# Optimization experiments

Measured on AMD Instinct MI355X. Metric: run time of the kernel, lower is better.

Reference implementation:

```python
import jax, jax.numpy as jnp
import numpy as np

N, E, F, H, G = 50000, 600000, 128, 128, 256
EPS = 1e-5
NEG_SLOPE = 0.2


def setup_inputs() -> dict:
    key = jax.random.key(0)
    ks = jax.random.split(key, 20)
    def w(k, shape, fan_in):
        return jax.random.normal(k, shape, jnp.float32) / np.sqrt(fan_in)
    x = jax.random.normal(ks[0], (N, F), jnp.float32)
    edge_index = jax.random.randint(ks[1], (2, E), 0, N, jnp.int32)
    batch = jnp.sort(jax.random.randint(ks[2], (N,), 0, G, jnp.int32))
    return {
        "x": x, "edge_index": edge_index, "batch": batch,
        "W1": w(ks[3], (F, H), F), "b1": jnp.zeros((H,), jnp.float32),
        "g1": jnp.ones((H,), jnp.float32), "be1": jnp.zeros((H,), jnp.float32),
        "Wg": w(ks[4], (H, H), H), "att_src": w(ks[5], (H,), H),
        "att_dst": w(ks[6], (H,), H), "bg": jnp.zeros((H,), jnp.float32),
        "g2": jnp.ones((H,), jnp.float32), "be2": jnp.zeros((H,), jnp.float32),
        "W3": w(ks[7], (H, H), H), "b3": jnp.zeros((H,), jnp.float32),
        "g3": jnp.ones((H,), jnp.float32), "be3": jnp.zeros((H,), jnp.float32),
        "fw1": w(ks[8], (H, H), H), "fb1": jnp.zeros((H,), jnp.float32),
        "fw2": w(ks[9], (H, 1), H), "fb2": jnp.zeros((1,), jnp.float32),
    }


def _with_self_loops(edge_index):
    loop = jnp.arange(N, dtype=edge_index.dtype)
    src = jnp.concatenate([edge_index[0], loop])
    dst = jnp.concatenate([edge_index[1], loop])
    return src, dst


def gcn_conv(x, W, b, src, dst):
    h = x @ W                                      # [N,H]
    deg = jax.ops.segment_sum(jnp.ones_like(dst, jnp.float32), dst, num_segments=N)
    dis = jnp.where(deg > 0, jax.lax.rsqrt(jnp.maximum(deg, 1.0)), 0.0)
    norm = dis[src] * dis[dst]                     # [E+N]
    msg = h[src] * norm[:, None]
    return jax.ops.segment_sum(msg, dst, num_segments=N) + b


def gat_conv(x, W, a_src, a_dst, b, src, dst):
    # single-head PyG GATConv with self loops
    h = x @ W                                      # [N,H]
    al_s = h @ a_src                               # [N]
    al_d = h @ a_dst
    e = jax.nn.leaky_relu(al_s[src] + al_d[dst], NEG_SLOPE)   # [E+N]
    m = jax.ops.segment_max(e, dst, num_segments=N)
    ex = jnp.exp(e - m[dst])
    denom = jax.ops.segment_sum(ex, dst, num_segments=N)
    alpha = ex / denom[dst]
    out = jax.ops.segment_sum(h[src] * alpha[:, None], dst, num_segments=N)
    return out + b


def batch_norm(x, gamma, beta):
    mu = jnp.mean(x, axis=0)
    var = jnp.var(x, axis=0)
    return gamma * (x - mu) * jax.lax.rsqrt(var + EPS) + beta


def reference(x, edge_index, batch, W1, b1, g1, be1, Wg, att_src, att_dst, bg,
              g2, be2, W3, b3, g3, be3, fw1, fb1, fw2, fb2):
    src, dst = _with_self_loops(edge_index)
    h = jax.nn.relu(batch_norm(gcn_conv(x, W1, b1, src, dst), g1, be1))
    # dropout = identity (eval mode)
    h = jax.nn.relu(batch_norm(gat_conv(h, Wg, att_src, att_dst, bg, src, dst), g2, be2))
    h = jax.nn.relu(batch_norm(gcn_conv(h, W3, b3, src, dst), g3, be3))
    # global mean pool over graphs
    sums = jax.ops.segment_sum(h, batch, num_segments=G)           # [G,H]
    cnts = jax.ops.segment_sum(jnp.ones((h.shape[0],), h.dtype), batch, num_segments=G)
    pooled = sums / jnp.maximum(cnts, 1.0)[:, None]
    z = jax.nn.relu(pooled @ fw1 + fb1)
    return z @ fw2 + fb2                                            # [G,1]
```

## Files before the change

### kernel.cpp

```cpp
#include <hip/hip_runtime.h>
#include <hip/hip_fp16.h>
#include <cstdint>

#define N_NODES 50000
#define N_EDGES 600000
#define HDIM    128
#define NGRAPH  256
#define EPSBN   1e-5f
#define NEG     0.2f
#define SCAN_B  196

__device__ __forceinline__ float lrelu(float v){ return v > 0.f ? v : NEG*v; }

typedef _Float16 f16x8 __attribute__((ext_vector_type(8)));
typedef float    f32x4 __attribute__((ext_vector_type(4)));

__global__ void prep_kernel(const float* __restrict__ W1, const float* __restrict__ Wg,
                            const float* __restrict__ W3, __half* __restrict__ Wt1,
                            __half* __restrict__ Wtg, __half* __restrict__ Wt3,
                            const int* __restrict__ ei, int* __restrict__ degi,
                            const int* __restrict__ batch, int* __restrict__ start){
  int b = blockIdx.x;
  if (b < 192){
    const float* W = (b < 64) ? W1 : (b < 128 ? Wg : W3);
    __half*     Wt = (b < 64) ? Wt1 : (b < 128 ? Wtg : Wt3);
    int idx = (b & 63)*256 + threadIdx.x;
    int k = idx >> 7, n = idx & 127;
    int kc = k >> 5, q = (k >> 3) & 3, j = k & 7;
    int nt = n >> 4, c16 = n & 15;
    Wt[(((kc*8 + nt)*4 + q)*16 + c16)*8 + j] = __float2half(W[idx]);
  } else if (b < 192 + 2344){
    int e = (b - 192)*256 + threadIdx.x;
    if (e < N_EDGES) atomicAdd(&degi[ei[N_EDGES + e]], 1);
  } else {
    int i = (b - 192 - 2344)*256 + threadIdx.x;
    if (i >= N_NODES) return;
    int bb = batch[i];
    int p = (i == 0) ? -1 : batch[i-1];
    for (int g = p+1; g <= bb; ++g) start[g] = i;
    if (i == N_NODES-1)
      for (int g = bb+1; g <= NGRAPH; ++g) start[g] = N_NODES;
  }
}

template<bool BN, bool F32IN, bool ATT, bool SCALE>
__global__ __launch_bounds__(256) void gemm_mfma(const void* __restrict__ Xv,
    const __half* __restrict__ Wt,
    const float* __restrict__ S, const float* __restrict__ Q,
    const float* __restrict__ gam, const float* __restrict__ bet,
    __half* __restrict__ Yh,
    const float* __restrict__ asr, const float* __restrict__ adt,
    float* __restrict__ al_s, float* __restrict__ al_d,
    const float* __restrict__ dis){
  __shared__ _Float16 scl[128], shl[128];
  const int t    = threadIdx.x;
  if (BN){
    if (t < 128){
      float mean = S[t] * (1.f/(float)N_NODES);
      float var  = fmaxf(Q[t]*(1.f/(float)N_NODES) - mean*mean, 0.f);
      float scale = gam[t]*rsqrtf(var + EPSBN);
      float shift = bet[t] - mean*scale;
      scl[t] = (_Float16)scale;
      shl[t] = (_Float16)shift;
    }
    __syncthreads();
  }
  const int wave = t >> 6, lane = t & 63;
  const int q    = lane >> 4, c16 = lane & 15;
  const int m0   = blockIdx.x*64 + wave*16;
  const int row  = m0 + c16;
  const int arow = (row > N_NODES-1) ? N_NODES-1 : row;

  f32x4 acc[8];
#pragma unroll
  for (int i = 0; i < 8; ++i) acc[i] = (f32x4){0.f,0.f,0.f,0.f};

  const f16x8* Wt8 = (const f16x8*)Wt;

#pragma unroll
  for (int kc = 0; kc < 4; ++kc){
    const int kof = kc*32 + q*8;
    f16x8 a;
    if (F32IN){
      const float* xp = (const float*)Xv + (long)arow*128 + kof;
      float4 x0 = *(const float4*)xp;
      float4 x1 = *(const float4*)(xp + 4);
      a[0]=(_Float16)x0.x; a[1]=(_Float16)x0.y; a[2]=(_Float16)x0.z; a[3]=(_Float16)x0.w;
      a[4]=(_Float16)x1.x; a[5]=(_Float16)x1.y; a[6]=(_Float16)x1.z; a[7]=(_Float16)x1.w;
    } else {
      f16x8 raw = *(const f16x8*)((const _Float16*)Xv + (long)arow*128 + kof);
      if (BN){
        f16x8 scv = *(const f16x8*)(scl + kof);
        f16x8 shv = *(const f16x8*)(shl + kof);
#pragma unroll
        for (int i = 0; i < 8; ++i){
          _Float16 v = (_Float16)(raw[i]*scv[i] + shv[i]);
          a[i] = v > (_Float16)0 ? v : (_Float16)0;
        }
      } else {
        a = raw;
      }
    }
#pragma unroll
    for (int nt = 0; nt < 8; ++nt){
      f16x8 b = Wt8[(kc*8 + nt)*64 + lane];
      acc[nt] = __builtin_amdgcn_mfma_f32_16x16x32_f16(b, a, acc[nt], 0, 0, 0);
    }
  }
  float rs = SCALE ? dis[arow] : 1.f;
  if (row < N_NODES){
    __half* yp = Yh + (long)row*128 + q*4;
#pragma unroll
    for (int nt = 0; nt < 8; ++nt){
      union { uint2 u; __half2 h[2]; } pk;
      pk.h[0] = __floats2half2_rn(acc[nt][0]*rs, acc[nt][1]*rs);
      pk.h[1] = __floats2half2_rn(acc[nt][2]*rs, acc[nt][3]*rs);
      *(uint2*)(yp + nt*16) = pk.u;
    }
  }
  if (ATT){
    float s = 0.f, d = 0.f;
#pragma unroll
    for (int nt = 0; nt < 8; ++nt){
      float4 av = *(const float4*)(asr + nt*16 + q*4);
      float4 bv = *(const float4*)(adt + nt*16 + q*4);
      s += acc[nt][0]*av.x + acc[nt][1]*av.y + acc[nt][2]*av.z + acc[nt][3]*av.w;
      d += acc[nt][0]*bv.x + acc[nt][1]*bv.y + acc[nt][2]*bv.z + acc[nt][3]*bv.w;
    }
    s += __shfl_xor(s, 16); s += __shfl_xor(s, 32);
    d += __shfl_xor(d, 16); d += __shfl_xor(d, 32);
    if (q == 0 && row < N_NODES){ al_s[row] = s; al_d[row] = d; }
  }
}

__global__ void scan_partial(const int* __restrict__ degi, int* __restrict__ part,
                             float* __restrict__ dis){
  __shared__ int sm[256];
  int t = threadIdx.x; int i = blockIdx.x*256 + t;
  int v = (i < N_NODES) ? degi[i] : 0;
  if (i < N_NODES) dis[i] = rsqrtf((float)v + 1.f);
  sm[t] = v;
  __syncthreads();
  for (int off = 128; off; off >>= 1){
    if (t < off) sm[t] += sm[t + off];
    __syncthreads();
  }
  if (t == 0) part[blockIdx.x] = sm[0];
}
__global__ void scan_final(const int* __restrict__ degi, const int* __restrict__ part,
                           int* __restrict__ rowp, int* __restrict__ work){
  __shared__ int sm[256];
  __shared__ int offs;
  int t = threadIdx.x; int i = blockIdx.x*256 + t;
  int pv = (t < SCAN_B && t < blockIdx.x) ? part[t] : 0;
  sm[t] = pv; __syncthreads();
  for (int off = 128; off; off >>= 1){
    if (t < off) sm[t] += sm[t + off];
    __syncthreads();
  }
  if (t == 0) offs = sm[0];
  __syncthreads();
  int v = (i < N_NODES) ? degi[i] : 0;
  sm[t] = v; __syncthreads();
  for (int off = 1; off < 256; off <<= 1){
    int add = (t >= off) ? sm[t - off] : 0;
    __syncthreads();
    sm[t] += add; __syncthreads();
  }
  if (i < N_NODES){
    int r = offs + sm[t] - v;
    rowp[i] = r;
    work[i] = r;
  }
}
__global__ void csr_scatter(const int* __restrict__ ei, int* __restrict__ work,
                            int* __restrict__ colx){
  int e = blockIdx.x*256 + threadIdx.x;
  if (e >= N_EDGES) return;
  int s = ei[e], d = ei[N_EDGES + e];
  int pos = atomicAdd(&work[d], 1);
  colx[pos] = s;
}

__global__ __launch_bounds__(256) void gcn_agg(const _Float16* __restrict__ Ah,
    const float* __restrict__ dis, const int* __restrict__ rowp,
    const int* __restrict__ degi, const int* __restrict__ colx,
    __half* __restrict__ Bh){
  const int n = blockIdx.x*4 + (threadIdx.x >> 6);
  const int lane = threadIdx.x & 63;
  const int g = lane >> 4, p = lane & 15;
  float acc[8] = {0,0,0,0,0,0,0,0};
  if (g == 0){
    f16x8 self = *(const f16x8*)(Ah + (long)n*128 + p*8);
#pragma unroll
    for (int i = 0; i < 8; ++i) acc[i] = (float)self[i];
  }
  const int e0 = rowp[n], cnt = degi[n];
  for (int base = 0; base < cnt; base += 64){
    int idx = base + lane;
    int s = 0; float w = 0.f;
    if (idx < cnt){ s = colx[e0 + idx]; w = 1.f; }
    int nit = min(64, cnt - base);
    int j = 0;
    for (; j + 8 <= nit; j += 8){
      int   s0 = __shfl(s, j + g),      s1 = __shfl(s, j + 4 + g);
      float w0 = __shfl(w, j + g),      w1 = __shfl(w, j + 4 + g);
      f16x8 r0 = *(const f16x8*)(Ah + (long)s0*128 + p*8);
      f16x8 r1 = *(const f16x8*)(Ah + (long)s1*128 + p*8);
#pragma unroll
      for (int i = 0; i < 8; ++i) acc[i] += w0 * (float)r0[i];
#pragma unroll
      for (int i = 0; i < 8; ++i) acc[i] += w1 * (float)r1[i];
    }
    for (; j < nit; j += 4){
      int   sj = __shfl(s, j + g);
      float wj = __shfl(w, j + g);
      f16x8 r = *(const f16x8*)(Ah + (long)sj*128 + p*8);
#pragma unroll
      for (int i = 0; i < 8; ++i) acc[i] += wj * (float)r[i];
    }
  }
#pragma unroll
  for (int i = 0; i < 8; ++i){
    acc[i] += __shfl_xor(acc[i], 16);
    acc[i] += __shfl_xor(acc[i], 32);
  }
  if (g == 0){
    float dn = dis[n];
    union { uint4 u; __half2 h[4]; } pk;
#pragma unroll
    for (int i = 0; i < 4; ++i)
      pk.h[i] = __floats2half2_rn(acc[2*i]*dn, acc[2*i+1]*dn);
    *(uint4*)(Bh + (long)n*128 + p*8) = pk.u;
  }
}

__global__ __launch_bounds__(256) void gat_agg(const _Float16* __restrict__ Ah,
    const float* __restrict__ al_s, const float* __restrict__ al_d,
    const int* __restrict__ rowp, const int* __restrict__ degi,
    const int* __restrict__ colx, __half* __restrict__ Bh){
  const int n = blockIdx.x*4 + (threadIdx.x >> 6);
  const int lane = threadIdx.x & 63;
  const int g = lane >> 4, p = lane & 15;
  const float adn = al_d[n];
  const float lself = lrelu(al_s[n] + adn);
  const int e0 = rowp[n], cnt = degi[n];
  int sReg = 0; float lv = -1e30f;
  if (lane < cnt){ sReg = colx[e0 + lane]; lv = lrelu(al_s[sReg] + adn); }
  float m = fmaxf(lself, lv);
  for (int base = 64; base < cnt; base += 64){
    int idx = base + lane;
    if (idx < cnt) m = fmaxf(m, lrelu(al_s[colx[e0 + idx]] + adn));
  }
#pragma unroll
  for (int off = 32; off; off >>= 1) m = fmaxf(m, __shfl_xor(m, off));
  const float exs = __expf(lself - m);
  float w = __expf(lv - m);
  float dpart = w;
  float acc[8] = {0,0,0,0,0,0,0,0};
  if (g == 0){
    f16x8 self = *(const f16x8*)(Ah + (long)n*128 + p*8);
#pragma unroll
    for (int i = 0; i < 8; ++i) acc[i] = exs * (float)self[i];
  }
  {
    int nit = min(64, cnt);
    int j = 0;
    for (; j + 8 <= nit; j += 8){
      int   s0 = __shfl(sReg, j + g),   s1 = __shfl(sReg, j + 4 + g);
      float w0 = __shfl(w,    j + g),   w1 = __shfl(w,    j + 4 + g);
      f16x8 r0 = *(const f16x8*)(Ah + (long)s0*128 + p*8);
      f16x8 r1 = *(const f16x8*)(Ah + (long)s1*128 + p*8);
#pragma unroll
      for (int i = 0; i < 8; ++i) acc[i] += w0 * (float)r0[i];
#pragma unroll
      for (int i = 0; i < 8; ++i) acc[i] += w1 * (float)r1[i];
    }
    for (; j < nit; j += 4){
      int   sj = __shfl(sReg, j + g);
      float wj = __shfl(w,    j + g);
      f16x8 r = *(const f16x8*)(Ah + (long)sj*128 + p*8);
#pragma unroll
      for (int i = 0; i < 8; ++i) acc[i] += wj * (float)r[i];
    }
  }
  for (int base = 64; base < cnt; base += 64){
    int idx = base + lane;
    int s2 = 0; float w2 = 0.f;
    if (idx < cnt){ s2 = colx[e0 + idx]; w2 = __expf(lrelu(al_s[s2] + adn) - m); }
    dpart += w2;
    int nit = min(64, cnt - base);
    for (int j = 0; j < nit; j += 4){
      int   sj = __shfl(s2, j + g);
      float wj = __shfl(w2, j + g);
      f16x8 r = *(const f16x8*)(Ah + (long)sj*128 + p*8);
#pragma unroll
      for (int i = 0; i < 8; ++i) acc[i] += wj * (float)r[i];
    }
  }
#pragma unroll
  for (int off = 32; off; off >>= 1) dpart += __shfl_xor(dpart, off);
#pragma unroll
  for (int i = 0; i < 8; ++i){
    acc[i] += __shfl_xor(acc[i], 16);
    acc[i] += __shfl_xor(acc[i], 32);
  }
  if (g == 0){
    float rinv = 1.f / (dpart + exs);
    union { uint4 u; __half2 h[4]; } pk;
#pragma unroll
    for (int i = 0; i < 4; ++i)
      pk.h[i] = __floats2half2_rn(acc[2*i]*rinv, acc[2*i+1]*rinv);
    *(uint4*)(Bh + (long)n*128 + p*8) = pk.u;
  }
}

__global__ void stats_h(const f16x8* __restrict__ X8,
                        float* __restrict__ S, float* __restrict__ Q){
  __shared__ float sb[16][16][8];
  __shared__ float qb[16][16][8];
  int t = threadIdx.x;
  int cg = t & 15, r = t >> 4;
  float s[8] = {0,0,0,0,0,0,0,0}, q[8] = {0,0,0,0,0,0,0,0};
  const int total = N_NODES*16;
  for (int idx = blockIdx.x*256 + t; idx < total; idx += gridDim.x*256){
    f16x8 v = X8[idx];
#pragma unroll
    for (int i = 0; i < 8; ++i){
      float f = (float)v[i];
      s[i] += f; q[i] += f*f;
    }
  }
#pragma unroll
  for (int i = 0; i < 8; ++i){ sb[r][cg][i] = s[i]; qb[r][cg][i] = q[i]; }
  __syncthreads();
  if (t < 128){
    int cg2 = t >> 3, j = t & 7;
    float as = 0.f, aq = 0.f;
#pragma unroll
    for (int r2 = 0; r2 < 16; ++r2){ as += sb[r2][cg2][j]; aq += qb[r2][cg2][j]; }
    atomicAdd(&S[cg2*8 + j], as);
    atomicAdd(&Q[cg2*8 + j], aq);
  }
}

__global__ void poolfinal(const __half* __restrict__ Bh, const int* __restrict__ start,
                          const float* __restrict__ S, const float* __restrict__ Q,
                          const float* __restrict__ gam, const float* __restrict__ bet,
                          const float* __restrict__ fw1, const float* __restrict__ fb1,
                          const float* __restrict__ fw2, const float* __restrict__ fb2,
                          float* __restrict__ out){
  __shared__ float scl[128], shl[128], psum[2][128], p[128], red[2];
  int t = threadIdx.x, gg = blockIdx.x;
  if (t < 128){
    float mean = S[t] * (1.f/(float)N_NODES);
    float var  = fmaxf(Q[t]*(1.f/(float)N_NODES) - mean*mean, 0.f);
    float scale = gam[t]*rsqrtf(var + EPSBN);
    scl[t] = scale;
    shl[t] = bet[t] - mean*scale;
  }
  __syncthreads();
  int s0 = start[gg], s1 = start[gg+1];
  int c = t & 127, h = t >> 7;
  float acc = 0.f;
  for (int n = s0 + h; n < s1; n += 2)
    acc += fmaxf(__half2float(Bh[(long)n*128 + c])*scl[c] + shl[c], 0.f);
  psum[h][c] = acc;
  __syncthreads();
  if (t < 128){
    float cnt = fmaxf((float)(s1 - s0), 1.f);
    p[t] = (psum[0][t] + psum[1][t]) / cnt;
  }
  __syncthreads();
  if (t < 128){
    float a = fb1[t];
    for (int k = 0; k < 128; ++k) a += p[k]*fw1[k*128 + t];
    float z = fmaxf(a, 0.f) * fw2[t];
    for (int off = 32; off; off >>= 1) z += __shfl_down(z, off);
    if ((t & 63) == 0) red[t >> 6] = z;
  }
  __syncthreads();
  if (t == 0) out[gg] = red[0] + red[1] + fb2[0];
}

extern "C" void kernel_launch(void* const* d_in, const int* in_sizes, int n_in,
                              void* d_out, int out_size, void* d_ws, size_t ws_size,
                              hipStream_t stream){
  const float* x    = (const float*)d_in[0];
  const int*   ei   = (const int*)d_in[1];
  const int*   batch= (const int*)d_in[2];
  const float* W1   = (const float*)d_in[3];
  const float* g1   = (const float*)d_in[5];
  const float* be1  = (const float*)d_in[6];
  const float* Wg   = (const float*)d_in[7];
  const float* asr  = (const float*)d_in[8];
  const float* adt  = (const float*)d_in[9];
  const float* g2   = (const float*)d_in[11];
  const float* be2  = (const float*)d_in[12];
  const float* W3   = (const float*)d_in[13];
  const float* g3   = (const float*)d_in[15];
  const float* be3  = (const float*)d_in[16];
  const float* fw1  = (const float*)d_in[17];
  const float* fb1  = (const float*)d_in[18];
  const float* fw2  = (const float*)d_in[19];
  const float* fb2  = (const float*)d_in[20];
  float* out = (float*)d_out;

  const long NH = (long)N_NODES*HDIM;
  __half* Ah    = (__half*)d_ws;
  __half* Bh    = Ah + NH;
  __half* Wt1   = Bh + NH;
  __half* Wtg   = Wt1 + 16384;
  __half* Wt3   = Wtg + 16384;
  float* dis    = (float*)(Wt3 + 16384);
  float* al_s   = dis + N_NODES;
  float* al_d   = al_s + N_NODES;
  int* deg_i    = (int*)(al_d + N_NODES);
  float* stats  = (float*)(deg_i + N_NODES);
  int* rowp     = (int*)(stats + 768);
  int* work     = rowp + N_NODES;
  int* colx     = work + N_NODES;
  int* start    = colx + N_EDGES;
  int* part     = start + NGRAPH + 1;

  hipMemsetAsync(deg_i, 0, (size_t)(N_NODES + 768) * sizeof(int), stream);

  const int TB = 256;
  const int gE  = (N_EDGES + TB - 1)/TB;
  const int gMM = (N_NODES + 63)/64;
  const int gAgg= N_NODES / 4;

  const _Float16* Ahf = (const _Float16*)Ah;
  const f16x8*    Bh8 = (const f16x8*)Bh;

  prep_kernel<<<192 + gE + SCAN_B, TB, 0, stream>>>(W1, Wg, W3, Wt1, Wtg, Wt3,
                                                    ei, deg_i, batch, start);
  scan_partial<<<SCAN_B, TB, 0, stream>>>(deg_i, part, dis);
  scan_final<<<SCAN_B, TB, 0, stream>>>(deg_i, part, rowp, work);
  csr_scatter<<<gE, TB, 0, stream>>>(ei, work, colx);

  gemm_mfma<false,true,false,true><<<gMM, TB, 0, stream>>>(x, Wt1,
      nullptr, nullptr, nullptr, nullptr, Ah, nullptr, nullptr, nullptr, nullptr, dis);
  gcn_agg<<<gAgg, TB, 0, stream>>>(Ahf, dis, rowp, deg_i, colx, Bh);
  stats_h<<<512, TB, 0, stream>>>(Bh8, stats + 0, stats + 128);

  gemm_mfma<true,false,true,false><<<gMM, TB, 0, stream>>>(Bh, Wtg,
      stats + 0, stats + 128, g1, be1, Ah, asr, adt, al_s, al_d, nullptr);
  gat_agg<<<gAgg, TB, 0, stream>>>(Ahf, al_s, al_d, rowp, deg_i, colx, Bh);
  stats_h<<<512, TB, 0, stream>>>(Bh8, stats + 256, stats + 384);

  gemm_mfma<true,false,false,true><<<gMM, TB, 0, stream>>>(Bh, Wt3,
      stats + 256, stats + 384, g2, be2, Ah, nullptr, nullptr, nullptr, nullptr, dis);
  gcn_agg<<<gAgg, TB, 0, stream>>>(Ahf, dis, rowp, deg_i, colx, Bh);
  stats_h<<<512, TB, 0, stream>>>(Bh8, stats + 512, stats + 640);

  poolfinal<<<NGRAPH, TB, 0, stream>>>(Bh, start, stats + 512, stats + 640, g3, be3,
                                       fw1, fb1, fw2, fb2, out);
}
```

Baseline: 377.9 us.

## Fuse BatchNorm statistics into aggregation kernels and merge degree scan

The GCN and GAT aggregation kernels become grid-stride loops over a fixed 1024-block grid. Each wave accumulates per-channel sum and sum-of-squares of its output rows, reduces them in shared memory and adds them into the global stats with atomics. This removes the three separate stats_h passes that re-read the fp16 activation matrix. The two-kernel degree scan is replaced by a single kernel whose blocks claim their offsets through an atomic counter, so CSR row ranges are contiguous but their block order is no longer deterministic. The stats are now taken from fp32 values before fp16 rounding, and the fixed grid may balance skewed degrees less evenly.

```diff
diff --git a/kernel.cpp b/kernel.cpp
--- a/kernel.cpp
+++ b/kernel.cpp
@@ -43,6 +43,37 @@
   }
 }
 
+__global__ void scan_kernel(const int* __restrict__ degi, int* __restrict__ rowp,
+                            int* __restrict__ work, float* __restrict__ dis,
+                            int* __restrict__ gctr){
+  __shared__ int sm[256];
+  __shared__ int base;
+  int t = threadIdx.x; int i = blockIdx.x*256 + t;
+  int v = (i < N_NODES) ? degi[i] : 0;
+  if (i < N_NODES) dis[i] = rsqrtf((float)v + 1.f);
+  sm[t] = v; __syncthreads();
+  for (int off = 1; off < 256; off <<= 1){
+    int add = (t >= off) ? sm[t - off] : 0;
+    __syncthreads();
+    sm[t] += add; __syncthreads();
+  }
+  if (t == 255) base = atomicAdd(gctr, sm[255]);
+  __syncthreads();
+  if (i < N_NODES){
+    int r = base + sm[t] - v;
+    rowp[i] = r;
+    work[i] = r;
+  }
+}
+__global__ void csr_scatter(const int* __restrict__ ei, int* __restrict__ work,
+                            int* __restrict__ colx){
+  int e = blockIdx.x*256 + threadIdx.x;
+  if (e >= N_EDGES) return;
+  int s = ei[e], d = ei[N_EDGES + e];
+  int pos = atomicAdd(&work[d], 1);
+  colx[pos] = s;
+}
+
 template<bool BN, bool F32IN, bool ATT, bool SCALE>
 __global__ __launch_bounds__(256) void gemm_mfma(const void* __restrict__ Xv,
     const __half* __restrict__ Wt,
@@ -133,214 +164,181 @@
   }
 }
 
-__global__ void scan_partial(const int* __restrict__ degi, int* __restrict__ part,
-                             float* __restrict__ dis){
-  __shared__ int sm[256];
-  int t = threadIdx.x; int i = blockIdx.x*256 + t;
-  int v = (i < N_NODES) ? degi[i] : 0;
-  if (i < N_NODES) dis[i] = rsqrtf((float)v + 1.f);
-  sm[t] = v;
-  __syncthreads();
-  for (int off = 128; off; off >>= 1){
-    if (t < off) sm[t] += sm[t + off];
-    __syncthreads();
-  }
-  if (t == 0) part[blockIdx.x] = sm[0];
-}
-__global__ void scan_final(const int* __restrict__ degi, const int* __restrict__ part,
-                           int* __restrict__ rowp, int* __restrict__ work){
-  __shared__ int sm[256];
-  __shared__ int offs;
-  int t = threadIdx.x; int i = blockIdx.x*256 + t;
-  int pv = (t < SCAN_B && t < blockIdx.x) ? part[t] : 0;
-  sm[t] = pv; __syncthreads();
-  for (int off = 128; off; off >>= 1){
-    if (t < off) sm[t] += sm[t + off];
-    __syncthreads();
-  }
-  if (t == 0) offs = sm[0];
-  __syncthreads();
-  int v = (i < N_NODES) ? degi[i] : 0;
-  sm[t] = v; __syncthreads();
-  for (int off = 1; off < 256; off <<= 1){
-    int add = (t >= off) ? sm[t - off] : 0;
-    __syncthreads();
-    sm[t] += add; __syncthreads();
-  }
-  if (i < N_NODES){
-    int r = offs + sm[t] - v;
-    rowp[i] = r;
-    work[i] = r;
-  }
-}
-__global__ void csr_scatter(const int* __restrict__ ei, int* __restrict__ work,
-                            int* __restrict__ colx){
-  int e = blockIdx.x*256 + threadIdx.x;
-  if (e >= N_EDGES) return;
-  int s = ei[e], d = ei[N_EDGES + e];
-  int pos = atomicAdd(&work[d], 1);
-  colx[pos] = s;
-}
+#define AGG_BLOCKS 1024
 
 __global__ __launch_bounds__(256) void gcn_agg(const _Float16* __restrict__ Ah,
     const float* __restrict__ dis, const int* __restrict__ rowp,
     const int* __restrict__ degi, const int* __restrict__ colx,
-    __half* __restrict__ Bh){
-  const int n = blockIdx.x*4 + (threadIdx.x >> 6);
-  const int lane = threadIdx.x & 63;
+    __half* __restrict__ Bh, float* __restrict__ Sg, float* __restrict__ Qg){
+  __shared__ float sb[4][128], qb[4][128];
+  const int wave = threadIdx.x >> 6, lane = threadIdx.x & 63;
   const int g = lane >> 4, p = lane & 15;
-  float acc[8] = {0,0,0,0,0,0,0,0};
+  float sacc[8] = {0,0,0,0,0,0,0,0}, qacc[8] = {0,0,0,0,0,0,0,0};
+
+  for (int n = blockIdx.x*4 + wave; n < N_NODES; n += AGG_BLOCKS*4){
+    float acc[8] = {0,0,0,0,0,0,0,0};
+    if (g == 0){
+      f16x8 self = *(const f16x8*)(Ah + (long)n*128 + p*8);
+#pragma unroll
+      for (int i = 0; i < 8; ++i) acc[i] = (float)self[i];
+    }
+    const int e0 = rowp[n], cnt = degi[n];
+    for (int base = 0; base < cnt; base += 64){
+      int idx = base + lane;
+      int s = 0; float w = 0.f;
+      if (idx < cnt){ s = colx[e0 + idx]; w = 1.f; }
+      int nit = min(64, cnt - base);
+      int j = 0;
+      for (; j + 8 <= nit; j += 8){
+        int   s0 = __shfl(s, j + g),      s1 = __shfl(s, j + 4 + g);
+        float w0 = __shfl(w, j + g),      w1 = __shfl(w, j + 4 + g);
+        f16x8 r0 = *(const f16x8*)(Ah + (long)s0*128 + p*8);
+        f16x8 r1 = *(const f16x8*)(Ah + (long)s1*128 + p*8);
+#pragma unroll
+        for (int i = 0; i < 8; ++i) acc[i] += w0 * (float)r0[i];
+#pragma unroll
+        for (int i = 0; i < 8; ++i) acc[i] += w1 * (float)r1[i];
+      }
+      for (; j < nit; j += 4){
+        int   sj = __shfl(s, j + g);
+        float wj = __shfl(w, j + g);
+        f16x8 r = *(const f16x8*)(Ah + (long)sj*128 + p*8);
+#pragma unroll
+        for (int i = 0; i < 8; ++i) acc[i] += wj * (float)r[i];
+      }
+    }
+#pragma unroll
+    for (int i = 0; i < 8; ++i){
+      acc[i] += __shfl_xor(acc[i], 16);
+      acc[i] += __shfl_xor(acc[i], 32);
+    }
+    if (g == 0){
+      float dn = dis[n];
+      union { uint4 u; __half2 h[4]; } pk;
+#pragma unroll
+      for (int i = 0; i < 4; ++i)
+        pk.h[i] = __floats2half2_rn(acc[2*i]*dn, acc[2*i+1]*dn);
+      *(uint4*)(Bh + (long)n*128 + p*8) = pk.u;
+#pragma unroll
+      for (int i = 0; i < 8; ++i){
+        float v = acc[i]*dn;
+        sacc[i] += v; qacc[i] += v*v;
+      }
+    }
+  }
   if (g == 0){
-    f16x8 self = *(const f16x8*)(Ah + (long)n*128 + p*8);
-#pragma unroll
-    for (int i = 0; i < 8; ++i) acc[i] = (float)self[i];
-  }
-  const int e0 = rowp[n], cnt = degi[n];
-  for (int base = 0; base < cnt; base += 64){
-    int idx = base + lane;
-    int s = 0; float w = 0.f;
-    if (idx < cnt){ s = colx[e0 + idx]; w = 1.f; }
-    int nit = min(64, cnt - base);
-    int j = 0;
-    for (; j + 8 <= nit; j += 8){
-      int   s0 = __shfl(s, j + g),      s1 = __shfl(s, j + 4 + g);
-      float w0 = __shfl(w, j + g),      w1 = __shfl(w, j + 4 + g);
-      f16x8 r0 = *(const f16x8*)(Ah + (long)s0*128 + p*8);
-      f16x8 r1 = *(const f16x8*)(Ah + (long)s1*128 + p*8);
-#pragma unroll
-      for (int i = 0; i < 8; ++i) acc[i] += w0 * (float)r0[i];
-#pragma unroll
-      for (int i = 0; i < 8; ++i) acc[i] += w1 * (float)r1[i];
-    }
-    for (; j < nit; j += 4){
-      int   sj = __shfl(s, j + g);
-      float wj = __shfl(w, j + g);
-      f16x8 r = *(const f16x8*)(Ah + (long)sj*128 + p*8);
-#pragma unroll
-      for (int i = 0; i < 8; ++i) acc[i] += wj * (float)r[i];
-    }
-  }
-#pragma unroll
-  for (int i = 0; i < 8; ++i){
-    acc[i] += __shfl_xor(acc[i], 16);
-    acc[i] += __shfl_xor(acc[i], 32);
-  }
-  if (g == 0){
-    float dn = dis[n];
-    union { uint4 u; __half2 h[4]; } pk;
-#pragma unroll
-    for (int i = 0; i < 4; ++i)
-      pk.h[i] = __floats2half2_rn(acc[2*i]*dn, acc[2*i+1]*dn);
-    *(uint4*)(Bh + (long)n*128 + p*8) = pk.u;
+#pragma unroll
+    for (int i = 0; i < 8; ++i){ sb[wave][p*8+i] = sacc[i]; qb[wave][p*8+i] = qacc[i]; }
+  }
+  __syncthreads();
+  int t = threadIdx.x;
+  if (t < 128){
+    float as = sb[0][t]+sb[1][t]+sb[2][t]+sb[3][t];
+    float aq = qb[0][t]+qb[1][t]+qb[2][t]+qb[3][t];
+    atomicAdd(&Sg[t], as);
+    atomicAdd(&Qg[t], aq);
   }
 }
 
 __global__ __launch_bounds__(256) void gat_agg(const _Float16* __restrict__ Ah,
     const float* __restrict__ al_s, const float* __restrict__ al_d,
     const int* __restrict__ rowp, const int* __restrict__ degi,
-    const int* __restrict__ colx, __half* __restrict__ Bh){
-  const int n = blockIdx.x*4 + (threadIdx.x >> 6);
-  const int lane = threadIdx.x & 63;
+    const int* __restrict__ colx, __half* __restrict__ Bh,
+    float* __restrict__ Sg, float* __restrict__ Qg){
+  __shared__ float sb[4][128], qb[4][128];
+  const int wave = threadIdx.x >> 6, lane = threadIdx.x & 63;
   const int g = lane >> 4, p = lane & 15;
-  const float adn = al_d[n];
-  const float lself = lrelu(al_s[n] + adn);
-  const int e0 = rowp[n], cnt = degi[n];
-  int sReg = 0; float lv = -1e30f;
-  if (lane < cnt){ sReg = colx[e0 + lane]; lv = lrelu(al_s[sReg] + adn); }
-  float m = fmaxf(lself, lv);
-  for (int base = 64; base < cnt; base += 64){
-    int idx = base + lane;
-    if (idx < cnt) m = fmaxf(m, lrelu(al_s[colx[e0 + idx]] + adn));
-  }
-#pragma unroll
-  for (int off = 32; off; off >>= 1) m = fmaxf(m, __shfl_xor(m, off));
-  const float exs = __expf(lself - m);
-  float w = __expf(lv - m);
-  float dpart = w;
-  float acc[8] = {0,0,0,0,0,0,0,0};
+  float sacc[8] = {0,0,0,0,0,0,0,0}, qacc[8] = {0,0,0,0,0,0,0,0};
+
+  for (int n = blockIdx.x*4 + wave; n < N_NODES; n += AGG_BLOCKS*4){
+    const float adn = al_d[n];
+    const float lself = lrelu(al_s[n] + adn);
+    const int e0 = rowp[n], cnt = degi[n];
+    int sReg = 0; float lv = -1e30f;
+    if (lane < cnt){ sReg = colx[e0 + lane]; lv = lrelu(al_s[sReg] + adn); }
+    float m = fmaxf(lself, lv);
+    for (int base = 64; base < cnt; base += 64){
+      int idx = base + lane;
+      if (idx < cnt) m = fmaxf(m, lrelu(al_s[colx[e0 + idx]] + adn));
+    }
+#pragma unroll
+    for (int off = 32; off; off >>= 1) m = fmaxf(m, __shfl_xor(m, off));
+    const float exs = __expf(lself - m);
+    float w = __expf(lv - m);
+    float dpart = w;
+    float acc[8] = {0,0,0,0,0,0,0,0};
+    if (g == 0){
+      f16x8 self = *(const f16x8*)(Ah + (long)n*128 + p*8);
+#pragma unroll
+      for (int i = 0; i < 8; ++i) acc[i] = exs * (float)self[i];
+    }
+    {
+      int nit = min(64, cnt);
+      int j = 0;
+      for (; j + 8 <= nit; j += 8){
+        int   s0 = __shfl(sReg, j + g),   s1 = __shfl(sReg, j + 4 + g);
+        float w0 = __shfl(w,    j + g),   w1 = __shfl(w,    j + 4 + g);
+        f16x8 r0 = *(const f16x8*)(Ah + (long)s0*128 + p*8);
+        f16x8 r1 = *(const f16x8*)(Ah + (long)s1*128 + p*8);
+#pragma unroll
+        for (int i = 0; i < 8; ++i) acc[i] += w0 * (float)r0[i];
+#pragma unroll
+        for (int i = 0; i < 8; ++i) acc[i] += w1 * (float)r1[i];
+      }
+      for (; j < nit; j += 4){
+        int   sj = __shfl(sReg, j + g);
+        float wj = __shfl(w,    j + g);
+        f16x8 r = *(const f16x8*)(Ah + (long)sj*128 + p*8);
+#pragma unroll
+        for (int i = 0; i < 8; ++i) acc[i] += wj * (float)r[i];
+      }
+    }
+    for (int base = 64; base < cnt; base += 64){
+      int idx = base + lane;
+      int s2 = 0; float w2 = 0.f;
+      if (idx < cnt){ s2 = colx[e0 + idx]; w2 = __expf(lrelu(al_s[s2] + adn) - m); }
+      dpart += w2;
+      int nit = min(64, cnt - base);
+      for (int j = 0; j < nit; j += 4){
+        int   sj = __shfl(s2, j + g);
+        float wj = __shfl(w2, j + g);
+        f16x8 r = *(const f16x8*)(Ah + (long)sj*128 + p*8);
+#pragma unroll
+        for (int i = 0; i < 8; ++i) acc[i] += wj * (float)r[i];
+      }
+    }
+#pragma unroll
+    for (int off = 32; off; off >>= 1) dpart += __shfl_xor(dpart, off);
+#pragma unroll
+    for (int i = 0; i < 8; ++i){
+      acc[i] += __shfl_xor(acc[i], 16);
+      acc[i] += __shfl_xor(acc[i], 32);
+    }
+    if (g == 0){
+      float rinv = 1.f / (dpart + exs);
+      union { uint4 u; __half2 h[4]; } pk;
+#pragma unroll
+      for (int i = 0; i < 4; ++i)
+        pk.h[i] = __floats2half2_rn(acc[2*i]*rinv, acc[2*i+1]*rinv);
+      *(uint4*)(Bh + (long)n*128 + p*8) = pk.u;
+#pragma unroll
+      for (int i = 0; i < 8; ++i){
+        float v = acc[i]*rinv;
+        sacc[i] += v; qacc[i] += v*v;
+      }
+    }
+  }
   if (g == 0){
-    f16x8 self = *(const f16x8*)(Ah + (long)n*128 + p*8);
-#pragma unroll
-    for (int i = 0; i < 8; ++i) acc[i] = exs * (float)self[i];
-  }
-  {
-    int nit = min(64, cnt);
-    int j = 0;
-    for (; j + 8 <= nit; j += 8){
-      int   s0 = __shfl(sReg, j + g),   s1 = __shfl(sReg, j + 4 + g);
-      float w0 = __shfl(w,    j + g),   w1 = __shfl(w,    j + 4 + g);
-      f16x8 r0 = *(const f16x8*)(Ah + (long)s0*128 + p*8);
-      f16x8 r1 = *(const f16x8*)(Ah + (long)s1*128 + p*8);
-#pragma unroll
-      for (int i = 0; i < 8; ++i) acc[i] += w0 * (float)r0[i];
-#pragma unroll
-      for (int i = 0; i < 8; ++i) acc[i] += w1 * (float)r1[i];
-    }
-    for (; j < nit; j += 4){
-      int   sj = __shfl(sReg, j + g);
-      float wj = __shfl(w,    j + g);
-      f16x8 r = *(const f16x8*)(Ah + (long)sj*128 + p*8);
-#pragma unroll
-      for (int i = 0; i < 8; ++i) acc[i] += wj * (float)r[i];
-    }
-  }
-  for (int base = 64; base < cnt; base += 64){
-    int idx = base + lane;
-    int s2 = 0; float w2 = 0.f;
-    if (idx < cnt){ s2 = colx[e0 + idx]; w2 = __expf(lrelu(al_s[s2] + adn) - m); }
-    dpart += w2;
-    int nit = min(64, cnt - base);
-    for (int j = 0; j < nit; j += 4){
-      int   sj = __shfl(s2, j + g);
-      float wj = __shfl(w2, j + g);
-      f16x8 r = *(const f16x8*)(Ah + (long)sj*128 + p*8);
-#pragma unroll
-      for (int i = 0; i < 8; ++i) acc[i] += wj * (float)r[i];
-    }
-  }
-#pragma unroll
-  for (int off = 32; off; off >>= 1) dpart += __shfl_xor(dpart, off);
-#pragma unroll
-  for (int i = 0; i < 8; ++i){
-    acc[i] += __shfl_xor(acc[i], 16);
-    acc[i] += __shfl_xor(acc[i], 32);
-  }
-  if (g == 0){
-    float rinv = 1.f / (dpart + exs);
-    union { uint4 u; __half2 h[4]; } pk;
-#pragma unroll
-    for (int i = 0; i < 4; ++i)
-      pk.h[i] = __floats2half2_rn(acc[2*i]*rinv, acc[2*i+1]*rinv);
-    *(uint4*)(Bh + (long)n*128 + p*8) = pk.u;
-  }
-}
-
-__global__ void stats_h(const f16x8* __restrict__ X8,
-                        float* __restrict__ S, float* __restrict__ Q){
-  __shared__ float sb[16][16][8];
-  __shared__ float qb[16][16][8];
+#pragma unroll
+    for (int i = 0; i < 8; ++i){ sb[wave][p*8+i] = sacc[i]; qb[wave][p*8+i] = qacc[i]; }
+  }
+  __syncthreads();
   int t = threadIdx.x;
-  int cg = t & 15, r = t >> 4;
-  float s[8] = {0,0,0,0,0,0,0,0}, q[8] = {0,0,0,0,0,0,0,0};
-  const int total = N_NODES*16;
-  for (int idx = blockIdx.x*256 + t; idx < total; idx += gridDim.x*256){
-    f16x8 v = X8[idx];
-#pragma unroll
-    for (int i = 0; i < 8; ++i){
-      float f = (float)v[i];
-      s[i] += f; q[i] += f*f;
-    }
-  }
-#pragma unroll
-  for (int i = 0; i < 8; ++i){ sb[r][cg][i] = s[i]; qb[r][cg][i] = q[i]; }
-  __syncthreads();
   if (t < 128){
-    int cg2 = t >> 3, j = t & 7;
-    float as = 0.f, aq = 0.f;
-#pragma unroll
-    for (int r2 = 0; r2 < 16; ++r2){ as += sb[r2][cg2][j]; aq += qb[r2][cg2][j]; }
-    atomicAdd(&S[cg2*8 + j], as);
-    atomicAdd(&Q[cg2*8 + j], aq);
+    float as = sb[0][t]+sb[1][t]+sb[2][t]+sb[3][t];
+    float aq = qb[0][t]+qb[1][t]+qb[2][t]+qb[3][t];
+    atomicAdd(&Sg[t], as);
+    atomicAdd(&Qg[t], aq);
   }
 }
 
@@ -417,42 +415,39 @@
   float* al_d   = al_s + N_NODES;
   int* deg_i    = (int*)(al_d + N_NODES);
   float* stats  = (float*)(deg_i + N_NODES);
-  int* rowp     = (int*)(stats + 768);
+  int* gctr     = (int*)(stats + 768);
+  int* rowp     = gctr + 4;
   int* work     = rowp + N_NODES;
   int* colx     = work + N_NODES;
   int* start    = colx + N_EDGES;
-  int* part     = start + NGRAPH + 1;
-
-  hipMemsetAsync(deg_i, 0, (size_t)(N_NODES + 768) * sizeof(int), stream);
+
+  hipMemsetAsync(deg_i, 0, (size_t)(N_NODES + 768 + 4) * sizeof(int), stream);
 
   const int TB = 256;
   const int gE  = (N_EDGES + TB - 1)/TB;
   const int gMM = (N_NODES + 63)/64;
-  const int gAgg= N_NODES / 4;
 
   const _Float16* Ahf = (const _Float16*)Ah;
-  const f16x8*    Bh8 = (const f16x8*)Bh;
 
   prep_kernel<<<192 + gE + SCAN_B, TB, 0, stream>>>(W1, Wg, W3, Wt1, Wtg, Wt3,
                                                     ei, deg_i, batch, start);
-  scan_partial<<<SCAN_B, TB, 0, stream>>>(deg_i, part, dis);
-  scan_final<<<SCAN_B, TB, 0, stream>>>(deg_i, part, rowp, work);
+  scan_kernel<<<SCAN_B, TB, 0, stream>>>(deg_i, rowp, work, dis, gctr);
   csr_scatter<<<gE, TB, 0, stream>>>(ei, work, colx);
 
   gemm_mfma<false,true,false,true><<<gMM, TB, 0, stream>>>(x, Wt1,
       nullptr, nullptr, nullptr, nullptr, Ah, nullptr, nullptr, nullptr, nullptr, dis);
-  gcn_agg<<<gAgg, TB, 0, stream>>>(Ahf, dis, rowp, deg_i, colx, Bh);
-  stats_h<<<512, TB, 0, stream>>>(Bh8, stats + 0, stats + 128);
+  gcn_agg<<<AGG_BLOCKS, TB, 0, stream>>>(Ahf, dis, rowp, deg_i, colx, Bh,
+                                         stats + 0, stats + 128);
 
   gemm_mfma<true,false,true,false><<<gMM, TB, 0, stream>>>(Bh, Wtg,
       stats + 0, stats + 128, g1, be1, Ah, asr, adt, al_s, al_d, nullptr);
-  gat_agg<<<gAgg, TB, 0, stream>>>(Ahf, al_s, al_d, rowp, deg_i, colx, Bh);
-  stats_h<<<512, TB, 0, stream>>>(Bh8, stats + 256, stats + 384);
+  gat_agg<<<AGG_BLOCKS, TB, 0, stream>>>(Ahf, al_s, al_d, rowp, deg_i, colx, Bh,
+                                         stats + 256, stats + 384);
 
   gemm_mfma<true,false,false,true><<<gMM, TB, 0, stream>>>(Bh, Wt3,
       stats + 256, stats + 384, g2, be2, Ah, nullptr, nullptr, nullptr, nullptr, dis);
-  gcn_agg<<<gAgg, TB, 0, stream>>>(Ahf, dis, rowp, deg_i, colx, Bh);
-  stats_h<<<512, TB, 0, stream>>>(Bh8, stats + 512, stats + 640);
+  gcn_agg<<<AGG_BLOCKS, TB, 0, stream>>>(Ahf, dis, rowp, deg_i, colx, Bh,
+                                         stats + 512, stats + 640);
 
   poolfinal<<<NGRAPH, TB, 0, stream>>>(Bh, start, stats + 512, stats + 640, g3, be3,
                                        fw1, fb1, fw2, fb2, out);
```

New measurement: 427.1 us. 13.0% more time.
